# Kernel optimization log

Hardware: AMD Instinct MI355X
Metric: run time of the kernel (lower is better)

## Reference

```python
import jax, jax.numpy as jnp
import numpy as np

B, MSTEP, NFEAT, ATT = 8192, 200, 64, 64

def setup_inputs() -> dict:
    key = jax.random.key(0)
    k1, k2, k3, k4, k5, k6 = jax.random.split(key, 6)
    sc_q = (6.0 / (NFEAT + ATT)) ** 0.5
    sc_s = (6.0 / (ATT + 1)) ** 0.5
    return {
        "x": jax.random.normal(k1, (B, NFEAT), dtype=jnp.float32),
        "mem": jax.random.normal(k2, (B, MSTEP, NFEAT), dtype=jnp.float32),
        "Wq": jax.random.uniform(k3, (NFEAT, ATT), jnp.float32, -sc_q, sc_q),
        "Wk": jax.random.uniform(k4, (NFEAT, ATT), jnp.float32, -sc_q, sc_q),
        "bias": jax.random.uniform(k5, (ATT,), jnp.float32, -sc_q, sc_q),
        "Ws": jax.random.uniform(k6, (ATT, 1), jnp.float32, -sc_s, sc_s),
    }

def reference(x, mem, Wq, Wk, bias, Ws):
    # query: [B, 1, att]
    query = (x @ Wq)[:, None, :]
    # key: [B, mstep, att]
    key = jnp.einsum("bmf,fa->bma", mem, Wk)
    # additive attention: tanh(q + k + b), scalar score, softmax over mstep
    proj = jnp.tanh(query + key + bias)
    scores = jnp.einsum("bma,ao->bm", proj, Ws)          # [B, mstep]
    weights = jax.nn.softmax(scores, axis=1)              # softmax over mstep
    # context: weighted sum of keys -> [B, att]
    context = jnp.einsum("bm,bma->ba", weights, key)
    return context
```

## Files before the change

kernel.cpp:

```cpp
#include <hip/hip_runtime.h>
#include <math.h>

#define MSTEP 200
#define NF 64
#define NA 64
#define NMT 13

typedef __bf16 bf16x8 __attribute__((ext_vector_type(8)));
typedef float  floatx4 __attribute__((ext_vector_type(4)));


__launch_bounds__(256, 3)
__global__ void customAttention_48515950576474_kernel(
    const float* __restrict__ x, const float* __restrict__ mem,
    const float* __restrict__ Wq, const float* __restrict__ Wk,
    const float* __restrict__ bias, const float* __restrict__ Ws,
    float* __restrict__ out)
{
    __shared__ __align__(16) __bf16 wh[NA * NF];
    __shared__ __align__(16) __bf16 wl[NA * NF];
    __shared__ float q_lds[NA];
    __shared__ float scores[NMT * 16];
    __shared__ float ctxp[4][NA];

    const int t    = threadIdx.x;
    const int b    = blockIdx.x;
    const int w    = t >> 6;
    const int lane = t & 63;

    const float* memb = mem + (size_t)b * (MSTEP * NF);

    for (int i = 0; i < 16; ++i) {
        int idx = t + (i << 8);
        int kk = idx >> 6, a = idx & 63;
        float v = Wk[idx];
        __bf16 hb = (__bf16)v;
        int eo = a * 64 + (((kk >> 3) ^ (a & 7)) << 3) + (kk & 7);
        wh[eo] = hb;
        wl[eo] = (__bf16)(v - (float)hb);
    }

    {
        float xv = x[(size_t)b * NF + lane];
        int aj = lane & 15, fh = lane >> 4;
        int a0 = w << 4;
        float qp = 0.f;
        #pragma unroll
        for (int kx = 0; kx < 16; ++kx) {
            int ff = fh * 16 + kx;
            qp = fmaf(__shfl(xv, ff), Wq[ff * NA + a0 + aj], qp);
        }
        qp += __shfl_xor(qp, 16);
        qp += __shfl_xor(qp, 32);
        if (fh == 0) q_lds[a0 + aj] = qp + bias[a0 + aj];
    }
    __syncthreads();

    bf16x8 bh[4][2], bl[4][2];
    {
        int a = lane & 15, ko = lane >> 4;
        #pragma unroll
        for (int at = 0; at < 4; ++at) {
            int row = at * 16 + a;
            #pragma unroll
            for (int kc = 0; kc < 2; ++kc) {
                int eo = row * 64 + ((((kc * 4 + ko)) ^ (row & 7)) << 3);
                bh[at][kc] = *(const bf16x8*)&wh[eo];
                bl[at][kc] = *(const bf16x8*)&wl[eo];
            }
        }
    }

    float qv[4], wsv[4];
    #pragma unroll
    for (int at = 0; at < 4; ++at) {
        int a = at * 16 + (lane & 15);
        qv[at]  = q_lds[a];
        wsv[at] = Ws[a];
    }

    floatx4 kreg[4][4];
    #pragma unroll
    for (int i = 0; i < 4; ++i)
        #pragma unroll
        for (int at = 0; at < 4; ++at)
            kreg[i][at] = (floatx4){0.f, 0.f, 0.f, 0.f};

    #pragma unroll
    for (int i = 0; i < 4; ++i) {
        int mt = w + 4 * i;
        if (mt < NMT) {
            int m  = mt * 16 + (lane & 15);
            int ko = lane >> 4;
            bool valid = (m < MSTEP);
            bf16x8 ah[2], al[2];
            #pragma unroll
            for (int kc = 0; kc < 2; ++kc) {
                const float* ap = memb + m * 64 + kc * 32 + ko * 8;
                float4 p0 = valid ? *(const float4*)ap       : make_float4(0.f, 0.f, 0.f, 0.f);
                float4 p1 = valid ? *(const float4*)(ap + 4) : make_float4(0.f, 0.f, 0.f, 0.f);
                float vv[8] = {p0.x, p0.y, p0.z, p0.w, p1.x, p1.y, p1.z, p1.w};
                bf16x8 h, l;
                #pragma unroll
                for (int j = 0; j < 8; ++j) {
                    __bf16 hb = (__bf16)vv[j];
                    h[j] = hb;
                    l[j] = (__bf16)(vv[j] - (float)hb);
                }
                ah[kc] = h;
                al[kc] = l;
            }
            #pragma unroll
            for (int at = 0; at < 4; ++at) {
                floatx4 acc = kreg[i][at];
                #pragma unroll
                for (int kc = 0; kc < 2; ++kc) {
                    acc = __builtin_amdgcn_mfma_f32_16x16x32_bf16(ah[kc], bh[at][kc], acc, 0, 0, 0);
                    acc = __builtin_amdgcn_mfma_f32_16x16x32_bf16(ah[kc], bl[at][kc], acc, 0, 0, 0);
                    acc = __builtin_amdgcn_mfma_f32_16x16x32_bf16(al[kc], bh[at][kc], acc, 0, 0, 0);
                }
                kreg[i][at] = acc;
            }
            float s[4] = {0.f, 0.f, 0.f, 0.f};
            #pragma unroll
            for (int at = 0; at < 4; ++at) {
                #pragma unroll
                for (int r = 0; r < 4; ++r) {
                    float e  = __expf(2.f * (kreg[i][at][r] + qv[at]));
                    float th = 1.f - 2.f / (e + 1.f);
                    s[r] = fmaf(th, wsv[at], s[r]);
                }
            }
            #pragma unroll
            for (int r = 0; r < 4; ++r) {
                s[r] += __shfl_xor(s[r], 1);
                s[r] += __shfl_xor(s[r], 2);
                s[r] += __shfl_xor(s[r], 4);
                s[r] += __shfl_xor(s[r], 8);
            }
            if ((lane & 15) == 0) {
                int mrow = mt * 16 + (lane >> 4) * 4;
                scores[mrow + 0] = s[0];
                scores[mrow + 1] = s[1];
                scores[mrow + 2] = s[2];
                scores[mrow + 3] = s[3];
            }
        }
    }
    __syncthreads();

    float mx, inv;
    {
        float s0 = scores[lane];
        float s1 = scores[lane + 64];
        float s2 = scores[lane + 128];
        float s3 = (lane < 8) ? scores[lane + 192] : -INFINITY;
        mx = fmaxf(fmaxf(s0, s1), fmaxf(s2, s3));
        #pragma unroll
        for (int d = 1; d < 64; d <<= 1) mx = fmaxf(mx, __shfl_xor(mx, d));
        float e = __expf(s0 - mx) + __expf(s1 - mx) + __expf(s2 - mx)
                + ((lane < 8) ? __expf(s3 - mx) : 0.f);
        #pragma unroll
        for (int d = 1; d < 64; d <<= 1) e += __shfl_xor(e, d);
        inv = 1.0f / e;
    }

    {
        float c[4] = {0.f, 0.f, 0.f, 0.f};
        #pragma unroll
        for (int i = 0; i < 4; ++i) {
            int mt = w + 4 * i;
            if (mt < NMT) {
                int mrow = mt * 16 + (lane >> 4) * 4;
                #pragma unroll
                for (int r = 0; r < 4; ++r) {
                    float wv = (mrow + r < MSTEP)
                             ? __expf(scores[mrow + r] - mx) * inv : 0.f;
                    #pragma unroll
                    for (int at = 0; at < 4; ++at)
                        c[at] = fmaf(wv, kreg[i][at][r], c[at]);
                }
            }
        }
        #pragma unroll
        for (int at = 0; at < 4; ++at) {
            c[at] += __shfl_xor(c[at], 16);
            c[at] += __shfl_xor(c[at], 32);
        }
        if (lane < 16) {
            #pragma unroll
            for (int at = 0; at < 4; ++at)
                ctxp[w][at * 16 + lane] = c[at];
        }
    }
    __syncthreads();

    if (t < NA)
        out[(size_t)b * NA + t] = ctxp[0][t] + ctxp[1][t] + ctxp[2][t] + ctxp[3][t];
}

extern "C" void kernel_launch(void* const* d_in, const int* in_sizes, int n_in,
                              void* d_out, int out_size, void* d_ws, size_t ws_size,
                              hipStream_t stream) {
    const float* x    = (const float*)d_in[0];
    const float* mem  = (const float*)d_in[1];
    const float* Wq   = (const float*)d_in[2];
    const float* Wk   = (const float*)d_in[3];
    const float* bias = (const float*)d_in[4];
    const float* Ws   = (const float*)d_in[5];
    float* out = (float*)d_out;
    const int B = in_sizes[0] / NF;
    customAttention_48515950576474_kernel<<<B, 256, 0, stream>>>(x, mem, Wq, Wk, bias, Ws, out);
}
```

Before: 589.3 us.

## Prefetch all memory rows into registers upfront and reload Wk fragments from LDS

```diff
diff --git a/kernel.cpp b/kernel.cpp
--- a/kernel.cpp
+++ b/kernel.cpp
@@ -30,6 +30,26 @@
 
     const float* memb = mem + (size_t)b * (MSTEP * NF);
 
+    float4 abuf[4][4];
+    #pragma unroll
+    for (int i = 0; i < 4; ++i) {
+        int mt = w + 4 * i;
+        int m  = mt * 16 + (lane & 15);
+        bool valid = (mt < NMT) && (m < MSTEP);
+        int mc = valid ? m : 0;
+        const float* ap = memb + mc * 64 + (lane >> 4) * 8;
+        #pragma unroll
+        for (int kc = 0; kc < 2; ++kc)
+            #pragma unroll
+            for (int h = 0; h < 2; ++h)
+                abuf[i][kc * 2 + h] = *(const float4*)(ap + kc * 32 + h * 4);
+        if (!valid) {
+            #pragma unroll
+            for (int p = 0; p < 4; ++p)
+                abuf[i][p] = make_float4(0.f, 0.f, 0.f, 0.f);
+        }
+    }
+
     for (int i = 0; i < 16; ++i) {
         int idx = t + (i << 8);
         int kk = idx >> 6, a = idx & 63;
@@ -56,21 +76,6 @@
     }
     __syncthreads();
 
-    bf16x8 bh[4][2], bl[4][2];
-    {
-        int a = lane & 15, ko = lane >> 4;
-        #pragma unroll
-        for (int at = 0; at < 4; ++at) {
-            int row = at * 16 + a;
-            #pragma unroll
-            for (int kc = 0; kc < 2; ++kc) {
-                int eo = row * 64 + ((((kc * 4 + ko)) ^ (row & 7)) << 3);
-                bh[at][kc] = *(const bf16x8*)&wh[eo];
-                bl[at][kc] = *(const bf16x8*)&wl[eo];
-            }
-        }
-    }
-
     float qv[4], wsv[4];
     #pragma unroll
     for (int at = 0; at < 4; ++at) {
@@ -90,15 +95,13 @@
     for (int i = 0; i < 4; ++i) {
         int mt = w + 4 * i;
         if (mt < NMT) {
-            int m  = mt * 16 + (lane & 15);
+            int a  = lane & 15;
             int ko = lane >> 4;
-            bool valid = (m < MSTEP);
             bf16x8 ah[2], al[2];
             #pragma unroll
             for (int kc = 0; kc < 2; ++kc) {
-                const float* ap = memb + m * 64 + kc * 32 + ko * 8;
-                float4 p0 = valid ? *(const float4*)ap       : make_float4(0.f, 0.f, 0.f, 0.f);
-                float4 p1 = valid ? *(const float4*)(ap + 4) : make_float4(0.f, 0.f, 0.f, 0.f);
+                float4 p0 = abuf[i][kc * 2 + 0];
+                float4 p1 = abuf[i][kc * 2 + 1];
                 float vv[8] = {p0.x, p0.y, p0.z, p0.w, p1.x, p1.y, p1.z, p1.w};
                 bf16x8 h, l;
                 #pragma unroll
@@ -112,12 +115,16 @@
             }
             #pragma unroll
             for (int at = 0; at < 4; ++at) {
+                int row = at * 16 + a;
                 floatx4 acc = kreg[i][at];
                 #pragma unroll
                 for (int kc = 0; kc < 2; ++kc) {
-                    acc = __builtin_amdgcn_mfma_f32_16x16x32_bf16(ah[kc], bh[at][kc], acc, 0, 0, 0);
-                    acc = __builtin_amdgcn_mfma_f32_16x16x32_bf16(ah[kc], bl[at][kc], acc, 0, 0, 0);
-                    acc = __builtin_amdgcn_mfma_f32_16x16x32_bf16(al[kc], bh[at][kc], acc, 0, 0, 0);
+                    int eo = row * 64 + (((kc * 4 + ko) ^ (row & 7)) << 3);
+                    bf16x8 bhx = *(const bf16x8*)&wh[eo];
+                    bf16x8 blx = *(const bf16x8*)&wl[eo];
+                    acc = __builtin_amdgcn_mfma_f32_16x16x32_bf16(ah[kc], bhx, acc, 0, 0, 0);
+                    acc = __builtin_amdgcn_mfma_f32_16x16x32_bf16(ah[kc], blx, acc, 0, 0, 0);
+                    acc = __builtin_amdgcn_mfma_f32_16x16x32_bf16(al[kc], bhx, acc, 0, 0, 0);
                 }
                 kreg[i][at] = acc;
             }
```

Result: faster. 577.5 us (-2.0%).
